# Kernel optimization log

Hardware: AMD Instinct MI355X
Metric: run time of the kernel (lower is better)

The kernel has to match this reference:

```python
import jax, jax.numpy as jnp
import numpy as np

# ---- config (JambaConfig defaults) ----
D_MODEL = 2048
D_STATE = 128
D_CONV = 4
EXPAND = 2
HEADDIM = 64
D_INNER = EXPAND * D_MODEL           # 4096
NHEADS = D_INNER // HEADDIM          # 64
CONV_DIM = D_INNER + 2 * D_STATE     # 4352
IN_PROJ = 2 * D_INNER + 2 * D_STATE + NHEADS  # 8512
INTER = 5632                         # ((2048*8/3)+255)//256*256
EPS = 1e-6
CHUNK = 128                          # SSD chunk length


def rmsnorm(x, w, eps=EPS):
    var = jnp.mean(jnp.square(x), axis=-1, keepdims=True)
    return x * jax.lax.rsqrt(var + eps) * w


def dw_causal_conv(x, w, b):
    # x: [B,L,C], w: [C,K] depthwise, b: [C]; causal (left pad K-1)
    xt = jnp.transpose(x, (0, 2, 1))                       # [B,C,L]
    xt = jnp.pad(xt, ((0, 0), (0, 0), (D_CONV - 1, 0)))
    y = jax.lax.conv_general_dilated(
        xt, w[:, None, :], window_strides=(1,), padding='VALID',
        feature_group_count=w.shape[0], dimension_numbers=('NCH', 'OIH', 'NCH'))
    y = y + b[None, :, None]
    return jnp.transpose(y, (0, 2, 1))                     # [B,L,C]


def segsum(x):
    # x: [..., T] -> [..., T, T] with out[l,s] = sum_{s<i<=l} x[i], -inf above diag
    T = x.shape[-1]
    xx = jnp.broadcast_to(x[..., None], (*x.shape, T))     # xx[...,i,j] = x[...,i]
    xx = jnp.where(jnp.tril(jnp.ones((T, T), bool), -1), xx, 0.0)
    s = jnp.cumsum(xx, axis=-2)
    return jnp.where(jnp.tril(jnp.ones((T, T), bool), 0), s, -jnp.inf)


def ssd(x, dt, A, Bm, Cm):
    # Mamba2 SSD (chunked selective scan). x:[b,l,h,p] dt:[b,l,h] A:[h] Bm/Cm:[b,l,n]
    b, l, h, p = x.shape
    n = Bm.shape[-1]
    c = l // CHUNK
    xr = x.reshape(b, c, CHUNK, h, p)
    dtr = dt.reshape(b, c, CHUNK, h)
    Br = Bm.reshape(b, c, CHUNK, n)
    Cr = Cm.reshape(b, c, CHUNK, n)
    dA = jnp.transpose(dtr * A, (0, 3, 1, 2))              # [b,h,c,q], all <= 0
    A_cum = jnp.cumsum(dA, axis=-1)                        # [b,h,c,q]
    L = jnp.exp(segsum(dA))                                # [b,h,c,q,q] lower-tri decays
    xdt = xr * dtr[..., None]                              # [b,c,q,h,p]
    # intra-chunk (diagonal blocks)
    Y_diag = jnp.einsum('bcln,bcsn,bhcls,bcshp->bclhp', Cr, Br, L, xdt)
    # chunk-final states
    decay_states = jnp.exp(A_cum[..., -1:] - A_cum)        # [b,h,c,q]
    states = jnp.einsum('bcln,bhcl,bclhp->bchpn', Br, decay_states, xdt)
    # inter-chunk recurrence (parallel via decay matrix over chunks)
    A_last = A_cum[..., -1]                                # [b,h,c]
    decay_chunk = jnp.exp(segsum(jnp.pad(A_last, ((0, 0), (0, 0), (1, 0)))))  # [b,h,c+1,c+1]
    states_cat = jnp.concatenate([jnp.zeros_like(states[:, :1]), states], axis=1)  # [b,c+1,h,p,n]
    new_states = jnp.einsum('bhzc,bchpn->bzhpn', decay_chunk, states_cat)
    prev = new_states[:, :-1]                              # state entering each chunk
    state_decay = jnp.exp(A_cum)                           # [b,h,c,q]
    Y_off = jnp.einsum('bcln,bchpn,bhcl->bclhp', Cr, prev, state_decay)
    return (Y_diag + Y_off).reshape(b, l, h, p)


def setup_inputs() -> dict:
    key = jax.random.key(0)
    ks = jax.random.split(key, 10)
    B, L = 2, 2048
    s = 0.02
    return {
        'hidden_states': jax.random.normal(ks[0], (B, L, D_MODEL), jnp.float32),
        'norm1_w': jnp.ones((D_MODEL,), jnp.float32),
        'in_proj_w': jax.random.normal(ks[1], (D_MODEL, IN_PROJ), jnp.float32) * s,
        'conv_w': jax.random.normal(ks[2], (CONV_DIM, D_CONV), jnp.float32) * 0.1,
        'conv_b': jnp.zeros((CONV_DIM,), jnp.float32),
        'dt_bias': jax.random.uniform(ks[3], (NHEADS,), jnp.float32, -4.0, -1.0),
        'A_log': jnp.log(jnp.arange(1, NHEADS + 1, dtype=jnp.float32)),
        'D_param': jnp.ones((NHEADS,), jnp.float32),
        'mixer_norm_w': jnp.ones((D_INNER,), jnp.float32),
        'out_proj_w': jax.random.normal(ks[4], (D_INNER, D_MODEL), jnp.float32) * s,
        'norm2_w': jnp.ones((D_MODEL,), jnp.float32),
        'gate_w': jax.random.normal(ks[5], (D_MODEL, INTER), jnp.float32) * s,
        'up_w': jax.random.normal(ks[6], (D_MODEL, INTER), jnp.float32) * s,
        'down_w': jax.random.normal(ks[7], (INTER, D_MODEL), jnp.float32) * s,
    }


def reference(hidden_states, norm1_w, in_proj_w, conv_w, conv_b, dt_bias, A_log,
              D_param, mixer_norm_w, out_proj_w, norm2_w, gate_w, up_w, down_w):
    B, L, _ = hidden_states.shape
    # --- norm1 + Mamba2 mixer + residual ---
    res = hidden_states
    h = rmsnorm(hidden_states, norm1_w)
    zxbcdt = h @ in_proj_w                                  # [B,L,8512]
    z = zxbcdt[..., :D_INNER]
    xBC = zxbcdt[..., D_INNER:D_INNER + CONV_DIM]
    dt = jax.nn.softplus(zxbcdt[..., -NHEADS:] + dt_bias)   # [B,L,H]
    xBC = jax.nn.silu(dw_causal_conv(xBC, conv_w, conv_b))
    xs = xBC[..., :D_INNER].reshape(B, L, NHEADS, HEADDIM)
    Bm = xBC[..., D_INNER:D_INNER + D_STATE]
    Cm = xBC[..., D_INNER + D_STATE:]
    A = -jnp.exp(A_log)
    y = ssd(xs, dt, A, Bm, Cm)
    y = y + D_param[None, None, :, None] * xs               # skip D term
    y = y.reshape(B, L, D_INNER)
    y = rmsnorm(y * jax.nn.silu(z), mixer_norm_w)           # gated RMSNorm
    h1 = res + y @ out_proj_w
    # --- norm2 + SwiGLU MLP + residual ---
    h2 = rmsnorm(h1, norm2_w)
    mlp = (jax.nn.silu(h2 @ gate_w) * (h2 @ up_w)) @ down_w
    return h1 + mlp
```

## Files before the change

### kernel.cpp

```cpp
#include <hip/hip_runtime.h>

#define LTOT 2048
#define BATCH 2
#define NTOK 4096
#define DMODEL 2048
#define DSTATE 128
#define NH 64
#define HD 64
#define DINNER 4096
#define CONVD 4352
#define XDTC 4416
#define INP 8512
#define INTER_ 5632
#define CHUNK_ 128
#define NCH 16
#define EPSF 1e-6f

typedef __bf16 bf16x8 __attribute__((ext_vector_type(8)));
typedef float f32x4 __attribute__((ext_vector_type(4)));
typedef unsigned short u16x4 __attribute__((ext_vector_type(4)));
typedef unsigned short u16x8 __attribute__((ext_vector_type(8)));

__device__ __forceinline__ unsigned short f2b(float f){
  unsigned int u = __builtin_bit_cast(unsigned int, f);
  u += 0x7fffu + ((u >> 16) & 1u);
  return (unsigned short)(u >> 16);
}
__device__ __forceinline__ float b2f(unsigned short h){
  return __builtin_bit_cast(float, ((unsigned int)h) << 16);
}
__device__ __forceinline__ f32x4 mfma16(bf16x8 a, bf16x8 b, f32x4 c){
  return __builtin_amdgcn_mfma_f32_16x16x32_bf16(a, b, c, 0, 0, 0);
}
typedef const __attribute__((address_space(1))) void* gas_t;
typedef __attribute__((address_space(3))) void* las_t;
__device__ __forceinline__ void gload16(const void* g, void* l){
  __builtin_amdgcn_global_load_lds((gas_t)g, (las_t)l, 16, 0, 0);
}

__global__ __launch_bounds__(256) void wconv_kernel(const float* __restrict__ W,
                                                    unsigned short* __restrict__ WT,
                                                    int K, int N)
{
  __shared__ unsigned short t[64][72];
  int n0 = blockIdx.x * 64, k0 = blockIdx.y * 64;
  int tid = threadIdx.x;
  int kl = tid >> 4, nl4 = (tid & 15) * 4;
  #pragma unroll
  for (int it = 0; it < 4; it++){
    int kk = kl + it * 16;
    float4 v = make_float4(0.f, 0.f, 0.f, 0.f);
    if (n0 < N) v = *(const float4*)&W[(size_t)(k0 + kk) * N + n0 + nl4];
    t[nl4 + 0][kk] = f2b(v.x);
    t[nl4 + 1][kk] = f2b(v.y);
    t[nl4 + 2][kk] = f2b(v.z);
    t[nl4 + 3][kk] = f2b(v.w);
  }
  __syncthreads();
  int nr = tid >> 3, k8 = (tid & 7) * 8;
  #pragma unroll
  for (int it = 0; it < 2; it++){
    int nn = nr + it * 32;
    *(u16x8*)&WT[(size_t)(n0 + nn) * K + k0 + k8] = *(const u16x8*)&t[nn][k8];
  }
}

__global__ __launch_bounds__(256) void rms_kernel(const float* __restrict__ x,
                                                  const float* __restrict__ w,
                                                  unsigned short* __restrict__ out, int width)
{
  int row = blockIdx.x, tid = threadIdx.x;
  const float* xr = x + (size_t)row * width;
  unsigned short* orow = out + (size_t)row * width;
  int nv = width >> 2;
  float ss = 0.f;
  for (int i = tid; i < nv; i += 256){
    float4 v = ((const float4*)xr)[i];
    ss += v.x*v.x + v.y*v.y + v.z*v.z + v.w*v.w;
  }
  #pragma unroll
  for (int off = 32; off > 0; off >>= 1) ss += __shfl_down(ss, off, 64);
  __shared__ float red[4];
  if ((tid & 63) == 0) red[tid >> 6] = ss;
  __syncthreads();
  float tot = red[0] + red[1] + red[2] + red[3];
  float scale = rsqrtf(tot / (float)width + EPSF);
  for (int i = tid; i < nv; i += 256){
    float4 v = ((const float4*)xr)[i];
    float4 wv = ((const float4*)w)[i];
    u16x4 o = { f2b(v.x * scale * wv.x), f2b(v.y * scale * wv.y),
                f2b(v.z * scale * wv.z), f2b(v.w * scale * wv.w) };
    ((u16x4*)orow)[i] = o;
  }
}

__global__ __launch_bounds__(256) void rms_gated_kernel(const float* __restrict__ y,
                                                        const unsigned short* __restrict__ z,
                                                        const float* __restrict__ w,
                                                        unsigned short* __restrict__ out)
{
  int row = blockIdx.x, tid = threadIdx.x;
  const float* yr = y + (size_t)row * DINNER;
  const unsigned short* zr = z + (size_t)row * DINNER;
  unsigned short* orow = out + (size_t)row * DINNER;
  float g[16];
  float ss = 0.f;
  #pragma unroll
  for (int ii = 0; ii < 4; ii++){
    int i = tid + ii * 256;
    float4 yv = ((const float4*)yr)[i];
    u16x4 zv = ((const u16x4*)zr)[i];
    #pragma unroll
    for (int e = 0; e < 4; e++){
      float zf = b2f(zv[e]);
      float yf = (&yv.x)[e];
      float gg = yf * (zf / (1.f + expf(-zf)));
      g[ii * 4 + e] = gg;
      ss += gg * gg;
    }
  }
  #pragma unroll
  for (int off = 32; off > 0; off >>= 1) ss += __shfl_down(ss, off, 64);
  __shared__ float red[4];
  if ((tid & 63) == 0) red[tid >> 6] = ss;
  __syncthreads();
  float tot = red[0] + red[1] + red[2] + red[3];
  float scale = rsqrtf(tot / (float)DINNER + EPSF);
  #pragma unroll
  for (int ii = 0; ii < 4; ii++){
    int i = tid + ii * 256;
    float4 wv = ((const float4*)w)[i];
    u16x4 o;
    #pragma unroll
    for (int e = 0; e < 4; e++) o[e] = f2b(g[ii * 4 + e] * scale * (&wv.x)[e]);
    ((u16x4*)orow)[i] = o;
  }
}

__global__ __launch_bounds__(512, 2) void gemm3_kernel(const unsigned short* __restrict__ A,
                                                       const unsigned short* __restrict__ BT,
                                                       const float* __restrict__ addsrc,
                                                       float* __restrict__ Cf,
                                                       unsigned short* __restrict__ Cb,
                                                       unsigned short* __restrict__ Cb2, int splitN,
                                                       const unsigned short* __restrict__ gate,
                                                       float* __restrict__ dtraw,
                                                       int M, int N, int K)
{
  extern __shared__ unsigned short lds[];
  int tid = threadIdx.x, lane = tid & 63, w = tid >> 6;
  int wm = w >> 2, wn = w & 3;
  int bid = blockIdx.x + blockIdx.y * gridDim.x;
  int nwg = gridDim.x * gridDim.y;
  int q8 = nwg >> 3, r8 = nwg & 7;
  int xcd = bid & 7, boff = bid >> 3;
  int wgid = (xcd < r8 ? xcd * (q8 + 1) : r8 * (q8 + 1) + (xcd - r8) * q8) + boff;
  int bn = (wgid % gridDim.x) * 256;
  int bm = (wgid / gridDim.x) * 128;

  int soct8 = ((lane & 3) ^ ((lane >> 2) & 3)) << 3;
  int prow_l = (lane >> 2);
  int ko = (((lane >> 4) ^ (lane & 3)) << 3);
  int rsel = (lane & 15) * 32 + ko;

  f32x4 acc[4][4] = {};
  int NT = K >> 5;

  #define STAGE(kt, bsel)                                                              \
    {                                                                                  \
      unsigned short* bb_ = &lds[(bsel) * 12288];                                      \
      size_t k0_ = (size_t)(kt) << 5;                                                  \
      gload16(&A [(size_t)(bm +       w * 16 + prow_l) * K + k0_ + soct8], &bb_[w * 512]);            \
      gload16(&BT[(size_t)(bn +       w * 16 + prow_l) * K + k0_ + soct8], &bb_[4096 + w * 512]);     \
      gload16(&BT[(size_t)(bn + 128 + w * 16 + prow_l) * K + k0_ + soct8], &bb_[8192 + w * 512]);     \
    }

  STAGE(0, 0)
  STAGE(1, 1)
  asm volatile("s_waitcnt vmcnt(3)" ::: "memory");
  __builtin_amdgcn_s_barrier();
  asm volatile("" ::: "memory");

  for (int t = 0; t < NT; ++t){
    const unsigned short* bufc = &lds[(t % 3) * 12288];
    bf16x8 afr[4], bfr[4];
    #pragma unroll
    for (int i = 0; i < 4; ++i)
      afr[i] = *(const bf16x8*)&bufc[(wm * 64 + i * 16) * 32 + rsel];
    #pragma unroll
    for (int c = 0; c < 4; ++c)
      bfr[c] = *(const bf16x8*)&bufc[4096 + (wn * 64 + c * 16) * 32 + rsel];
    if (t + 2 < NT) STAGE(t + 2, (t + 2) % 3)
    asm volatile("" ::: "memory");
    __builtin_amdgcn_s_barrier();
    asm volatile("s_waitcnt lgkmcnt(0)" ::: "memory");
    __builtin_amdgcn_s_setprio(1);
    #pragma unroll
    for (int i = 0; i < 4; ++i)
      #pragma unroll
      for (int c = 0; c < 4; ++c)
        acc[i][c] = mfma16(afr[i], bfr[c], acc[i][c]);
    __builtin_amdgcn_s_setprio(0);
    if (t + 2 < NT)      asm volatile("s_waitcnt vmcnt(3)" ::: "memory");
    else if (t + 1 < NT) asm volatile("s_waitcnt vmcnt(0)" ::: "memory");
    asm volatile("" ::: "memory");
    __builtin_amdgcn_s_barrier();
    asm volatile("" ::: "memory");
  }
  #undef STAGE

  int r0 = bm + wm * 64 + ((lane >> 4) << 2);
  int c0 = bn + wn * 64 + (lane & 15);
  #pragma unroll
  for (int i = 0; i < 4; ++i){
    #pragma unroll
    for (int j = 0; j < 4; ++j){
      int cc = c0 + j * 16;
      if (cc < N){
        #pragma unroll
        for (int e = 0; e < 4; ++e){
          int rr = r0 + i * 16 + e;
          float v = acc[i][j][e];
          if (Cf){
            size_t idx = (size_t)rr * N + cc;
            if (addsrc) v += addsrc[idx];
            Cf[idx] = v;
          } else if (cc < splitN){
            size_t idx = (size_t)rr * splitN + cc;
            float vv = v;
            if (gate){ float gg = b2f(gate[idx]); vv = gg / (1.f + expf(-gg)) * v; }
            Cb[idx] = f2b(vv);
          } else {
            Cb2[(size_t)rr * (N - splitN) + (cc - splitN)] = f2b(v);
            if (dtraw && cc >= N - NH) dtraw[(size_t)rr * NH + (cc - (N - NH))] = v;
          }
        }
      }
    }
  }
}

__global__ __launch_bounds__(256) void dt_kernel(const float* __restrict__ dtraw,
                                                 const float* __restrict__ dt_bias,
                                                 float* __restrict__ dtb)
{
  int idx = blockIdx.x * 256 + threadIdx.x;
  float raw = dtraw[idx] + dt_bias[idx & 63];
  dtb[idx] = (raw > 20.f) ? raw : log1pf(expf(raw));
}

__global__ __launch_bounds__(64) void acum_kernel(const float* __restrict__ dtb,
                                                  const float* __restrict__ A_log,
                                                  float* __restrict__ acum)
{
  int bid = blockIdx.x;
  int c = bid & 15;
  int hh = (bid >> 4) & 63;
  int b = bid >> 10;
  int lane = threadIdx.x;
  float Av = -expf(A_log[hh]);
  int rowbase = b * LTOT + c * CHUNK_;
  float v0 = dtb[(size_t)(rowbase + 2 * lane) * NH + hh] * Av;
  float v1 = dtb[(size_t)(rowbase + 2 * lane + 1) * NH + hh] * Av;
  float s = v0 + v1;
  #pragma unroll
  for (int d = 1; d < 64; d <<= 1){
    float t = __shfl_up(s, d, 64);
    if (lane >= d) s += t;
  }
  float excl = s - (v0 + v1);
  float* dst = acum + ((size_t)(b * NH + hh)) * LTOT + c * CHUNK_;
  dst[2 * lane]     = excl + v0;
  dst[2 * lane + 1] = excl + v0 + v1;
}

__global__ __launch_bounds__(256) void conv_kernel(const unsigned short* __restrict__ xdt,
                                                   const float* __restrict__ cw,
                                                   const float* __restrict__ cb,
                                                   unsigned short* __restrict__ xbc)
{
  int ch = blockIdx.x * 256 + threadIdx.x;
  int l = blockIdx.y, b = blockIdx.z;
  float acc = cb[ch];
  #pragma unroll
  for (int j = 0; j < 4; j++){
    int ls = l + j - 3;
    if (ls >= 0) acc += b2f(xdt[((size_t)(b * LTOT + ls)) * XDTC + ch]) * cw[ch * 4 + j];
  }
  acc = acc / (1.f + expf(-acc));
  xbc[((size_t)(b * LTOT + l)) * CONVD + ch] = f2b(acc);
}

__global__ __launch_bounds__(256) void ssd_sy_kernel(const unsigned short* __restrict__ xbc,
                                                     const float* __restrict__ dtb,
                                                     const float* __restrict__ acum,
                                                     float* __restrict__ y)
{
  int hh = blockIdx.x;
  int c = blockIdx.y >> 1;
  int half = blockIdx.y & 1;
  int b = blockIdx.z;
  __shared__ unsigned short Cs[64][136];
  __shared__ unsigned short Bs[128][136];
  __shared__ float ac[128];
  int tid = threadIdx.x, lane = tid & 63, w = tid >> 6;
  int l0 = half * 64;
  size_t rowbase = (size_t)b * LTOT + c * CHUNK_;
  if (tid < 128) ac[tid] = acum[((size_t)(b * NH + hh)) * LTOT + c * CHUNK_ + tid];
  #pragma unroll
  for (int p = 0; p < 8; p++){
    int lr = p * 8 + (tid >> 5);
    int n4 = (tid & 31) * 4;
    *(u16x4*)&Cs[lr][n4] =
      *(const u16x4*)&xbc[(rowbase + l0 + lr) * CONVD + DINNER + DSTATE + n4];
  }
  #pragma unroll
  for (int p = 0; p < 16; p++){
    int s = p * 8 + (tid >> 5);
    int n4 = (tid & 31) * 4;
    *(u16x4*)&Bs[s][n4] = *(const u16x4*)&xbc[(rowbase + s) * CONVD + DINNER + n4];
  }
  __syncthreads();
  f32x4 accS[8] = {};
  #pragma unroll
  for (int kk = 0; kk < 4; kk++){
    bf16x8 a = *(const bf16x8*)&Cs[w * 16 + (lane & 15)][kk * 32 + (lane >> 4) * 8];
    #pragma unroll
    for (int fc = 0; fc < 8; fc++){
      bf16x8 bb = *(const bf16x8*)&Bs[fc * 16 + (lane & 15)][kk * 32 + (lane >> 4) * 8];
      accS[fc] = mfma16(a, bb, accS[fc]);
    }
  }
  __syncthreads();
  {
    int lr = w * 16 + ((lane >> 4) << 2);
    #pragma unroll
    for (int fc = 0; fc < 8; fc++){
      int s = fc * 16 + (lane & 15);
      #pragma unroll
      for (int j = 0; j < 4; j++){
        int l = l0 + lr + j;
        float v = (s <= l) ? accS[fc][j] * expf(ac[l] - ac[s]) : 0.f;
        Cs[lr + j][s] = f2b(v);
      }
    }
  }
  #pragma unroll
  for (int p = 0; p < 8; p++){
    int lr = p * 16 + (tid >> 4);
    int p4 = (tid & 15) * 4;
    float dtl = dtb[(rowbase + lr) * NH + hh];
    u16x4 v = *(const u16x4*)&xbc[(rowbase + lr) * CONVD + hh * HD + p4];
    Bs[p4 + 0][lr] = f2b(b2f(v[0]) * dtl);
    Bs[p4 + 1][lr] = f2b(b2f(v[1]) * dtl);
    Bs[p4 + 2][lr] = f2b(b2f(v[2]) * dtl);
    Bs[p4 + 3][lr] = f2b(b2f(v[3]) * dtl);
  }
  __syncthreads();
  f32x4 accY[4] = {};
  #pragma unroll
  for (int kk = 0; kk < 4; kk++){
    bf16x8 a = *(const bf16x8*)&Cs[w * 16 + (lane & 15)][kk * 32 + (lane >> 4) * 8];
    #pragma unroll
    for (int fc = 0; fc < 4; fc++){
      bf16x8 bb = *(const bf16x8*)&Bs[fc * 16 + (lane & 15)][kk * 32 + (lane >> 4) * 8];
      accY[fc] = mfma16(a, bb, accY[fc]);
    }
  }
  {
    int lr = w * 16 + ((lane >> 4) << 2);
    #pragma unroll
    for (int fc = 0; fc < 4; fc++){
      int p = fc * 16 + (lane & 15);
      #pragma unroll
      for (int j = 0; j < 4; j++){
        y[(rowbase + l0 + lr + j) * DINNER + hh * HD + p] = accY[fc][j];
      }
    }
  }
}

__global__ __launch_bounds__(256) void ssd_states_kernel(const unsigned short* __restrict__ xbc,
                                                         const float* __restrict__ dtb,
                                                         const float* __restrict__ acum,
                                                         unsigned short* __restrict__ states)
{
  int hh = blockIdx.x, c = blockIdx.y, b = blockIdx.z;
  __shared__ unsigned short BsT[128][136];
  __shared__ unsigned short XT[64][136];
  __shared__ float ac[128];
  int tid = threadIdx.x, lane = tid & 63, w = tid >> 6;
  size_t rowbase = (size_t)b * LTOT + c * CHUNK_;
  if (tid < 128) ac[tid] = acum[((size_t)(b * NH + hh)) * LTOT + c * CHUNK_ + tid];
  #pragma unroll
  for (int p = 0; p < 16; p++){
    int l = p * 8 + (tid >> 5);
    int n4 = (tid & 31) * 4;
    u16x4 v = *(const u16x4*)&xbc[(rowbase + l) * CONVD + DINNER + n4];
    BsT[n4 + 0][l] = v[0];
    BsT[n4 + 1][l] = v[1];
    BsT[n4 + 2][l] = v[2];
    BsT[n4 + 3][l] = v[3];
  }
  #pragma unroll
  for (int p = 0; p < 8; p++){
    int l = p * 16 + (tid >> 4);
    int p4 = (tid & 15) * 4;
    float dtl = dtb[(rowbase + l) * NH + hh];
    u16x4 v = *(const u16x4*)&xbc[(rowbase + l) * CONVD + hh * HD + p4];
    XT[p4 + 0][l] = f2b(b2f(v[0]) * dtl);
    XT[p4 + 1][l] = f2b(b2f(v[1]) * dtl);
    XT[p4 + 2][l] = f2b(b2f(v[2]) * dtl);
    XT[p4 + 3][l] = f2b(b2f(v[3]) * dtl);
  }
  __syncthreads();
  float aclast = ac[127];
  f32x4 accP[8] = {};
  #pragma unroll
  for (int kk = 0; kk < 4; kk++){
    int kbase = kk * 32 + (lane >> 4) * 8;
    union { u16x4 q[2]; unsigned short u[8]; bf16x8 v; } rw, ot;
    rw.q[0] = *(const u16x4*)&XT[w * 16 + (lane & 15)][kbase];
    rw.q[1] = *(const u16x4*)&XT[w * 16 + (lane & 15)][kbase + 4];
    #pragma unroll
    for (int e = 0; e < 8; e++){
      ot.u[e] = f2b(b2f(rw.u[e]) * expf(aclast - ac[kbase + e]));
    }
    #pragma unroll
    for (int fc = 0; fc < 8; fc++){
      bf16x8 bb = *(const bf16x8*)&BsT[fc * 16 + (lane & 15)][kbase];
      accP[fc] = mfma16(ot.v, bb, accP[fc]);
    }
  }
  size_t sbase = ((size_t)((b * NCH + c) * NH + hh)) * HD * DSTATE;
  int p0 = w * 16 + ((lane >> 4) << 2);
  #pragma unroll
  for (int fc = 0; fc < 8; fc++){
    int n = fc * 16 + (lane & 15);
    #pragma unroll
    for (int j = 0; j < 4; j++){
      states[sbase + (size_t)(p0 + j) * DSTATE + n] = f2b(accP[fc][j]);
    }
  }
}

__global__ __launch_bounds__(256) void scan_kernel(unsigned short* __restrict__ states,
                                                   const float* __restrict__ acum)
{
  int bh = blockIdx.x;
  int b = bh >> 6, hh = bh & 63;
  int t = threadIdx.x;
  float run[32];
  #pragma unroll
  for (int j = 0; j < 32; j++) run[j] = 0.f;
  for (int c = 0; c < NCH; c++){
    float alast = acum[(size_t)bh * LTOT + c * CHUNK_ + 127];
    float dec = expf(alast);
    size_t base = ((size_t)((b * NCH + c) * NH + hh)) * (HD * DSTATE);
    #pragma unroll
    for (int j = 0; j < 32; j++){
      size_t idx = base + (size_t)j * 256 + t;
      float sc = b2f(states[idx]);
      states[idx] = f2b(run[j]);
      run[j] = run[j] * dec + sc;
    }
  }
}

__global__ __launch_bounds__(256) void ssd3_kernel(const unsigned short* __restrict__ xbc,
                                                   const unsigned short* __restrict__ states,
                                                   const float* __restrict__ acum,
                                                   const float* __restrict__ Dp,
                                                   float* __restrict__ y)
{
  int hh = blockIdx.x, c = blockIdx.y, b = blockIdx.z;
  __shared__ unsigned short Cs[128][136];
  __shared__ unsigned short Ps[64][136];
  __shared__ float ac[128];
  int tid = threadIdx.x, lane = tid & 63, w = tid >> 6;
  size_t rowbase = (size_t)b * LTOT + c * CHUNK_;
  if (tid < 128) ac[tid] = acum[((size_t)(b * NH + hh)) * LTOT + c * CHUNK_ + tid];
  #pragma unroll
  for (int p = 0; p < 16; p++){
    int l = p * 8 + (tid >> 5);
    int n4 = (tid & 31) * 4;
    *(u16x4*)&Cs[l][n4] =
      *(const u16x4*)&xbc[(rowbase + l) * CONVD + DINNER + DSTATE + n4];
  }
  size_t sbase = ((size_t)((b * NCH + c) * NH + hh)) * (HD * DSTATE);
  #pragma unroll
  for (int p = 0; p < 8; p++){
    int pp = p * 8 + (tid >> 5);
    int n4 = (tid & 31) * 4;
    *(u16x4*)&Ps[pp][n4] = *(const u16x4*)&states[sbase + (size_t)pp * DSTATE + n4];
  }
  __syncthreads();
  f32x4 acc[2][4] = {};
  #pragma unroll
  for (int kk = 0; kk < 4; kk++){
    bf16x8 a0 = *(const bf16x8*)&Cs[w * 32 + (lane & 15)][kk * 32 + (lane >> 4) * 8];
    bf16x8 a1 = *(const bf16x8*)&Cs[w * 32 + 16 + (lane & 15)][kk * 32 + (lane >> 4) * 8];
    #pragma unroll
    for (int fc = 0; fc < 4; fc++){
      bf16x8 bb = *(const bf16x8*)&Ps[fc * 16 + (lane & 15)][kk * 32 + (lane >> 4) * 8];
      acc[0][fc] = mfma16(a0, bb, acc[0][fc]);
      acc[1][fc] = mfma16(a1, bb, acc[1][fc]);
    }
  }
  float dpar = Dp[hh];
  #pragma unroll
  for (int fr = 0; fr < 2; fr++){
    int lr = w * 32 + fr * 16 + ((lane >> 4) << 2);
    #pragma unroll
    for (int fc = 0; fc < 4; fc++){
      int p = fc * 16 + (lane & 15);
      #pragma unroll
      for (int j = 0; j < 4; j++){
        int l = lr + j;
        size_t yi = (rowbase + l) * DINNER + hh * HD + p;
        float xsv = b2f(xbc[(rowbase + l) * CONVD + hh * HD + p]);
        y[yi] += acc[fr][fc][j] * expf(ac[l]) + dpar * xsv;
      }
    }
  }
}

extern "C" void kernel_launch(void* const* d_in, const int* in_sizes, int n_in,
                              void* d_out, int out_size, void* d_ws, size_t ws_size,
                              hipStream_t stream)
{
  (void)in_sizes; (void)n_in; (void)out_size; (void)ws_size;
  const float* hidden    = (const float*)d_in[0];
  const float* norm1_w   = (const float*)d_in[1];
  const float* in_proj_w = (const float*)d_in[2];
  const float* conv_w    = (const float*)d_in[3];
  const float* conv_b    = (const float*)d_in[4];
  const float* dt_bias   = (const float*)d_in[5];
  const float* A_log     = (const float*)d_in[6];
  const float* D_param   = (const float*)d_in[7];
  const float* mixer_w   = (const float*)d_in[8];
  const float* out_proj_w= (const float*)d_in[9];
  const float* norm2_w   = (const float*)d_in[10];
  const float* gate_w    = (const float*)d_in[11];
  const float* up_w      = (const float*)d_in[12];
  const float* down_w    = (const float*)d_in[13];

  char* ws = (char*)d_ws;
  unsigned short* zbuf    = (unsigned short*)(ws);
  unsigned short* WT_gate = (unsigned short*)(ws);
  unsigned short* xdt     = (unsigned short*)(ws + 33554432ull);
  unsigned short* states  = (unsigned short*)(ws + 33554432ull);
  unsigned short* ygn     = (unsigned short*)(ws + 33554432ull);
  unsigned short* WT_up   = (unsigned short*)(ws + 33554432ull);
  unsigned short* xbc     = (unsigned short*)(ws + 69730304ull);
  unsigned short* WT_out  = (unsigned short*)(ws + 69730304ull);
  unsigned short* h2      = (unsigned short*)(ws + 69730304ull);
  unsigned short* WT_down = (unsigned short*)(ws + 69730304ull);
  float* dtraw            = (float*)(ws + 105381888ull);
  float* dtb              = (float*)(ws + 106430464ull);
  float* acum             = (float*)(ws + 107479040ull);
  float* ybuf             = (float*)(ws + 108527616ull);
  unsigned short* hbuf    = (unsigned short*)(ws + 108527616ull);
  unsigned short* gbuf    = (unsigned short*)(ws + 108527616ull);
  unsigned short* WT_in   = (unsigned short*)(ws + 125304832ull);
  float* h1               = (float*)d_out;
  float* outp             = (float*)d_out;

  const int dynLDS = 73728;
  hipFuncSetAttribute((const void*)gemm3_kernel,
                      hipFuncAttributeMaxDynamicSharedMemorySize, dynLDS);

  wconv_kernel<<<dim3(136, 32), 256, 0, stream>>>(in_proj_w, WT_in, DMODEL, INP);
  rms_kernel<<<NTOK, 256, 0, stream>>>(hidden, norm1_w, hbuf, DMODEL);
  gemm3_kernel<<<dim3(34, 32), 512, dynLDS, stream>>>(hbuf, WT_in, nullptr, nullptr,
                                                      zbuf, xdt, DINNER, nullptr, dtraw,
                                                      NTOK, INP, DMODEL);
  dt_kernel<<<NTOK * NH / 256, 256, 0, stream>>>(dtraw, dt_bias, dtb);
  acum_kernel<<<BATCH * NH * NCH, 64, 0, stream>>>(dtb, A_log, acum);
  conv_kernel<<<dim3(CONVD / 256, LTOT, BATCH), 256, 0, stream>>>(xdt, conv_w, conv_b, xbc);
  ssd_sy_kernel<<<dim3(NH, NCH * 2, BATCH), 256, 0, stream>>>(xbc, dtb, acum, ybuf);
  ssd_states_kernel<<<dim3(NH, NCH, BATCH), 256, 0, stream>>>(xbc, dtb, acum, states);
  scan_kernel<<<BATCH * NH, 256, 0, stream>>>(states, acum);
  ssd3_kernel<<<dim3(NH, NCH, BATCH), 256, 0, stream>>>(xbc, states, acum, D_param, ybuf);
  rms_gated_kernel<<<NTOK, 256, 0, stream>>>(ybuf, zbuf, mixer_w, ygn);
  wconv_kernel<<<dim3(32, 64), 256, 0, stream>>>(out_proj_w, WT_out, DINNER, DMODEL);
  gemm3_kernel<<<dim3(8, 32), 512, dynLDS, stream>>>(ygn, WT_out, hidden, h1,
                                                     nullptr, nullptr, 0, nullptr, nullptr,
                                                     NTOK, DMODEL, DINNER);
  rms_kernel<<<NTOK, 256, 0, stream>>>(h1, norm2_w, h2, DMODEL);
  wconv_kernel<<<dim3(88, 32), 256, 0, stream>>>(gate_w, WT_gate, DMODEL, INTER_);
  gemm3_kernel<<<dim3(22, 32), 512, dynLDS, stream>>>(h2, WT_gate, nullptr, nullptr,
                                                      gbuf, nullptr, INTER_, nullptr, nullptr,
                                                      NTOK, INTER_, DMODEL);
  wconv_kernel<<<dim3(88, 32), 256, 0, stream>>>(up_w, WT_up, DMODEL, INTER_);
  gemm3_kernel<<<dim3(22, 32), 512, dynLDS, stream>>>(h2, WT_up, nullptr, nullptr,
                                                      gbuf, nullptr, INTER_, gbuf, nullptr,
                                                      NTOK, INTER_, DMODEL);
  wconv_kernel<<<dim3(32, 88), 256, 0, stream>>>(down_w, WT_down, INTER_, DMODEL);
  gemm3_kernel<<<dim3(8, 32), 512, dynLDS, stream>>>(gbuf, WT_down, h1, outp,
                                                     nullptr, nullptr, 0, nullptr, nullptr,
                                                     NTOK, DMODEL, INTER_);
}
```

Measured before the change: 1.088 ms.

## Add 128x128 GEMM for N=2048 projections, batch conv rows, parallelize scan, drop barrier

Adds a 256-thread gemm4 kernel with 128x128 tiles and a smaller LDS footprint for the out_proj and down_proj GEMMs. Those have N=2048, so the grid grows from 256 to 512 workgroups, which should fill the CUs better. The conv kernel now computes 4 consecutive rows per thread and reuses the overlapping loads. The state scan is split across 8 blocks per head, cutting registers per thread and adding parallelism. One mid-loop barrier in gemm3 is also removed, which risks a race on the LDS buffer being refilled while other waves still read it.

Measured after the change: 1.036 ms. 1.05x faster.

```diff
diff --git a/kernel.cpp b/kernel.cpp
--- a/kernel.cpp
+++ b/kernel.cpp
@@ -191,8 +191,6 @@
     for (int c = 0; c < 4; ++c)
       bfr[c] = *(const bf16x8*)&bufc[4096 + (wn * 64 + c * 16) * 32 + rsel];
     if (t + 2 < NT) STAGE(t + 2, (t + 2) % 3)
-    asm volatile("" ::: "memory");
-    __builtin_amdgcn_s_barrier();
     asm volatile("s_waitcnt lgkmcnt(0)" ::: "memory");
     __builtin_amdgcn_s_setprio(1);
     #pragma unroll
@@ -240,6 +238,92 @@
   }
 }
 
+__global__ __launch_bounds__(256, 3) void gemm4_kernel(const unsigned short* __restrict__ A,
+                                                       const unsigned short* __restrict__ BT,
+                                                       const float* __restrict__ addsrc,
+                                                       float* __restrict__ Cf,
+                                                       int M, int N, int K)
+{
+  extern __shared__ unsigned short lds[];
+  int tid = threadIdx.x, lane = tid & 63, w = tid >> 6;
+  int wm = w >> 1, wn = w & 1;
+  int bid = blockIdx.x + blockIdx.y * gridDim.x;
+  int nwg = gridDim.x * gridDim.y;
+  int q8 = nwg >> 3, r8 = nwg & 7;
+  int xcd = bid & 7, boff = bid >> 3;
+  int wgid = (xcd < r8 ? xcd * (q8 + 1) : r8 * (q8 + 1) + (xcd - r8) * q8) + boff;
+  int bn = (wgid % gridDim.x) * 128;
+  int bm = (wgid / gridDim.x) * 128;
+
+  int soct8 = ((lane & 3) ^ ((lane >> 2) & 3)) << 3;
+  int prow_l = (lane >> 2);
+  int ko = (((lane >> 4) ^ (lane & 3)) << 3);
+  int rsel = (lane & 15) * 32 + ko;
+
+  f32x4 acc[4][4] = {};
+  int NT = K >> 5;
+
+  #define STAGE4(kt, bsel)                                                             \
+    {                                                                                  \
+      unsigned short* bb_ = &lds[(bsel) * 8192];                                       \
+      size_t k0_ = (size_t)(kt) << 5;                                                  \
+      gload16(&A [(size_t)(bm +      w * 16 + prow_l) * K + k0_ + soct8], &bb_[w * 512]);          \
+      gload16(&A [(size_t)(bm + 64 + w * 16 + prow_l) * K + k0_ + soct8], &bb_[2048 + w * 512]);   \
+      gload16(&BT[(size_t)(bn +      w * 16 + prow_l) * K + k0_ + soct8], &bb_[4096 + w * 512]);   \
+      gload16(&BT[(size_t)(bn + 64 + w * 16 + prow_l) * K + k0_ + soct8], &bb_[6144 + w * 512]);   \
+    }
+
+  STAGE4(0, 0)
+  STAGE4(1, 1)
+  asm volatile("s_waitcnt vmcnt(4)" ::: "memory");
+  __builtin_amdgcn_s_barrier();
+  asm volatile("" ::: "memory");
+
+  for (int t = 0; t < NT; ++t){
+    const unsigned short* bufc = &lds[(t % 3) * 8192];
+    bf16x8 afr[4], bfr[4];
+    #pragma unroll
+    for (int i = 0; i < 4; ++i)
+      afr[i] = *(const bf16x8*)&bufc[(wm * 64 + i * 16) * 32 + rsel];
+    #pragma unroll
+    for (int c = 0; c < 4; ++c)
+      bfr[c] = *(const bf16x8*)&bufc[4096 + (wn * 64 + c * 16) * 32 + rsel];
+    if (t + 2 < NT) STAGE4(t + 2, (t + 2) % 3)
+    asm volatile("s_waitcnt lgkmcnt(0)" ::: "memory");
+    __builtin_amdgcn_s_setprio(1);
+    #pragma unroll
+    for (int i = 0; i < 4; ++i)
+      #pragma unroll
+      for (int c = 0; c < 4; ++c)
+        acc[i][c] = mfma16(afr[i], bfr[c], acc[i][c]);
+    __builtin_amdgcn_s_setprio(0);
+    if (t + 2 < NT)      asm volatile("s_waitcnt vmcnt(4)" ::: "memory");
+    else if (t + 1 < NT) asm volatile("s_waitcnt vmcnt(0)" ::: "memory");
+    asm volatile("" ::: "memory");
+    __builtin_amdgcn_s_barrier();
+    asm volatile("" ::: "memory");
+  }
+  #undef STAGE4
+
+  int r0 = bm + wm * 64 + ((lane >> 4) << 2);
+  int c0 = bn + wn * 64 + (lane & 15);
+  #pragma unroll
+  for (int i = 0; i < 4; ++i){
+    #pragma unroll
+    for (int j = 0; j < 4; ++j){
+      int cc = c0 + j * 16;
+      #pragma unroll
+      for (int e = 0; e < 4; ++e){
+        int rr = r0 + i * 16 + e;
+        size_t idx = (size_t)rr * N + cc;
+        float v = acc[i][j][e];
+        if (addsrc) v += addsrc[idx];
+        Cf[idx] = v;
+      }
+    }
+  }
+}
+
 __global__ __launch_bounds__(256) void dt_kernel(const float* __restrict__ dtraw,
                                                  const float* __restrict__ dt_bias,
                                                  float* __restrict__ dtb)
@@ -280,15 +364,21 @@
                                                    unsigned short* __restrict__ xbc)
 {
   int ch = blockIdx.x * 256 + threadIdx.x;
-  int l = blockIdx.y, b = blockIdx.z;
-  float acc = cb[ch];
-  #pragma unroll
-  for (int j = 0; j < 4; j++){
-    int ls = l + j - 3;
-    if (ls >= 0) acc += b2f(xdt[((size_t)(b * LTOT + ls)) * XDTC + ch]) * cw[ch * 4 + j];
-  }
-  acc = acc / (1.f + expf(-acc));
-  xbc[((size_t)(b * LTOT + l)) * CONVD + ch] = f2b(acc);
+  int l0 = blockIdx.y * 4, b = blockIdx.z;
+  float x[7];
+  #pragma unroll
+  for (int j = 0; j < 7; j++){
+    int ls = l0 - 3 + j;
+    x[j] = (ls >= 0) ? b2f(xdt[((size_t)(b * LTOT + ls)) * XDTC + ch]) : 0.f;
+  }
+  float w0 = cw[ch * 4 + 0], w1 = cw[ch * 4 + 1], w2 = cw[ch * 4 + 2], w3 = cw[ch * 4 + 3];
+  float bias = cb[ch];
+  #pragma unroll
+  for (int i = 0; i < 4; i++){
+    float acc = bias + x[i] * w0 + x[i + 1] * w1 + x[i + 2] * w2 + x[i + 3] * w3;
+    acc = acc / (1.f + expf(-acc));
+    xbc[((size_t)(b * LTOT + l0 + i)) * CONVD + ch] = f2b(acc);
+  }
 }
 
 __global__ __launch_bounds__(256) void ssd_sy_kernel(const unsigned short* __restrict__ xbc,
@@ -449,17 +539,16 @@
 {
   int bh = blockIdx.x;
   int b = bh >> 6, hh = bh & 63;
+  int jg = blockIdx.y * 4;
   int t = threadIdx.x;
-  float run[32];
-  #pragma unroll
-  for (int j = 0; j < 32; j++) run[j] = 0.f;
+  float run[4] = {0.f, 0.f, 0.f, 0.f};
   for (int c = 0; c < NCH; c++){
     float alast = acum[(size_t)bh * LTOT + c * CHUNK_ + 127];
     float dec = expf(alast);
     size_t base = ((size_t)((b * NCH + c) * NH + hh)) * (HD * DSTATE);
     #pragma unroll
-    for (int j = 0; j < 32; j++){
-      size_t idx = base + (size_t)j * 256 + t;
+    for (int j = 0; j < 4; j++){
+      size_t idx = base + (size_t)(jg + j) * 256 + t;
       float sc = b2f(states[idx]);
       states[idx] = f2b(run[j]);
       run[j] = run[j] * dec + sc;
@@ -566,38 +655,39 @@
   float* h1               = (float*)d_out;
   float* outp             = (float*)d_out;
 
-  const int dynLDS = 73728;
+  const int dynLDS3 = 73728;
+  const int dynLDS4 = 49152;
   hipFuncSetAttribute((const void*)gemm3_kernel,
-                      hipFuncAttributeMaxDynamicSharedMemorySize, dynLDS);
+                      hipFuncAttributeMaxDynamicSharedMemorySize, dynLDS3);
+  hipFuncSetAttribute((const void*)gemm4_kernel,
+                      hipFuncAttributeMaxDynamicSharedMemorySize, dynLDS4);
 
   wconv_kernel<<<dim3(136, 32), 256, 0, stream>>>(in_proj_w, WT_in, DMODEL, INP);
   rms_kernel<<<NTOK, 256, 0, stream>>>(hidden, norm1_w, hbuf, DMODEL);
-  gemm3_kernel<<<dim3(34, 32), 512, dynLDS, stream>>>(hbuf, WT_in, nullptr, nullptr,
-                                                      zbuf, xdt, DINNER, nullptr, dtraw,
-                                                      NTOK, INP, DMODEL);
+  gemm3_kernel<<<dim3(34, 32), 512, dynLDS3, stream>>>(hbuf, WT_in, nullptr, nullptr,
+                                                       zbuf, xdt, DINNER, nullptr, dtraw,
+                                                       NTOK, INP, DMODEL);
   dt_kernel<<<NTOK * NH / 256, 256, 0, stream>>>(dtraw, dt_bias, dtb);
   acum_kernel<<<BATCH * NH * NCH, 64, 0, stream>>>(dtb, A_log, acum);
-  conv_kernel<<<dim3(CONVD / 256, LTOT, BATCH), 256, 0, stream>>>(xdt, conv_w, conv_b, xbc);
+  conv_kernel<<<dim3(CONVD / 256, LTOT / 4, BATCH), 256, 0, stream>>>(xdt, conv_w, conv_b, xbc);
   ssd_sy_kernel<<<dim3(NH, NCH * 2, BATCH), 256, 0, stream>>>(xbc, dtb, acum, ybuf);
   ssd_states_kernel<<<dim3(NH, NCH, BATCH), 256, 0, stream>>>(xbc, dtb, acum, states);
-  scan_kernel<<<BATCH * NH, 256, 0, stream>>>(states, acum);
+  scan_kernel<<<dim3(BATCH * NH, 8), 256, 0, stream>>>(states, acum);
   ssd3_kernel<<<dim3(NH, NCH, BATCH), 256, 0, stream>>>(xbc, states, acum, D_param, ybuf);
   rms_gated_kernel<<<NTOK, 256, 0, stream>>>(ybuf, zbuf, mixer_w, ygn);
   wconv_kernel<<<dim3(32, 64), 256, 0, stream>>>(out_proj_w, WT_out, DINNER, DMODEL);
-  gemm3_kernel<<<dim3(8, 32), 512, dynLDS, stream>>>(ygn, WT_out, hidden, h1,
-                                                     nullptr, nullptr, 0, nullptr, nullptr,
-                                                     NTOK, DMODEL, DINNER);
+  gemm4_kernel<<<dim3(16, 32), 256, dynLDS4, stream>>>(ygn, WT_out, hidden, h1,
+                                                       NTOK, DMODEL, DINNER);
   rms_kernel<<<NTOK, 256, 0, stream>>>(h1, norm2_w, h2, DMODEL);
   wconv_kernel<<<dim3(88, 32), 256, 0, stream>>>(gate_w, WT_gate, DMODEL, INTER_);
-  gemm3_kernel<<<dim3(22, 32), 512, dynLDS, stream>>>(h2, WT_gate, nullptr, nullptr,
-                                                      gbuf, nullptr, INTER_, nullptr, nullptr,
-                                                      NTOK, INTER_, DMODEL);
+  gemm3_kernel<<<dim3(22, 32), 512, dynLDS3, stream>>>(h2, WT_gate, nullptr, nullptr,
+                                                       gbuf, nullptr, INTER_, nullptr, nullptr,
+                                                       NTOK, INTER_, DMODEL);
   wconv_kernel<<<dim3(88, 32), 256, 0, stream>>>(up_w, WT_up, DMODEL, INTER_);
-  gemm3_kernel<<<dim3(22, 32), 512, dynLDS, stream>>>(h2, WT_up, nullptr, nullptr,
-                                                      gbuf, nullptr, INTER_, gbuf, nullptr,
-                                                      NTOK, INTER_, DMODEL);
+  gemm3_kernel<<<dim3(22, 32), 512, dynLDS3, stream>>>(h2, WT_up, nullptr, nullptr,
+                                                       gbuf, nullptr, INTER_, gbuf, nullptr,
+                                                       NTOK, INTER_, DMODEL);
   wconv_kernel<<<dim3(32, 88), 256, 0, stream>>>(down_w, WT_down, INTER_, DMODEL);
-  gemm3_kernel<<<dim3(8, 32), 512, dynLDS, stream>>>(gbuf, WT_down, h1, outp,
-                                                     nullptr, nullptr, 0, nullptr, nullptr,
-                                                     NTOK, DMODEL, INTER_);
-}
+  gemm4_kernel<<<dim3(16, 32), 256, dynLDS4, stream>>>(gbuf, WT_down, h1, outp,
+                                                       NTOK, DMODEL, INTER_);
+}
```
